# Performance work log

Hardware: AMD Instinct MI355X
Metric: run time of the kernel (lower is better)

Reference implementation:

```python
import jax, jax.numpy as jnp
import numpy as np
from jax import lax

# NARX hyperparameters (match init_kwargs)
D_I, D_O, D_X, D_Y, D_HL = 8, 8, 32, 16, 256
B, T = 2048, 512
IN_SIZE = D_I * D_X + D_O * D_Y  # 384


def setup_inputs() -> dict:
    key = jax.random.key(0)
    k1, k2, k3, k4, k5 = jax.random.split(key, 5)
    s1 = 1.0 / np.sqrt(IN_SIZE).astype(np.float32)
    s2 = 1.0 / np.sqrt(D_HL).astype(np.float32)
    x = jax.random.normal(k1, (B, T, D_X), dtype=jnp.float32)
    W1 = jax.random.uniform(k2, (D_HL, IN_SIZE), jnp.float32, -s1, s1)
    b1 = jax.random.uniform(k3, (D_HL,), jnp.float32, -s1, s1)
    W2 = jax.random.uniform(k4, (D_Y, D_HL), jnp.float32, -s2, s2)
    b2 = jax.random.uniform(k5, (D_Y,), jnp.float32, -s2, s2)
    return {"x": x, "W1": W1, "b1": b1, "W2": W2, "b2": b2}


def reference(x, W1, b1, W2, b2):
    # Closed-loop NARX: mode='close', y=None, bootstrap=None.
    # y_pred starts as zeros; loop runs from max(d_i, d_o) to T.
    Bb, Tt, _ = x.shape
    start = max(D_I, D_O)

    def step(hist, t):
        # hist: [B, d_o, d_y], oldest first == y_pred[:, t-d_o:t, :]
        xw = lax.dynamic_slice_in_dim(x, t - D_I, D_I, axis=1).reshape(Bb, D_I * D_X)
        inp = jnp.concatenate([xw, hist.reshape(Bb, D_O * D_Y)], axis=1)
        h = jnp.tanh(inp @ W1.T + b1)
        out = jax.nn.sigmoid(h @ W2.T + b2)  # act2 = Sigmoid
        new_hist = jnp.concatenate([hist[:, 1:, :], out[:, None, :]], axis=1)
        return new_hist, out

    hist0 = jnp.zeros((Bb, D_O, D_Y), dtype=x.dtype)  # zero-initialized y_pred history
    _, outs = lax.scan(step, hist0, jnp.arange(start, Tt))
    outs = jnp.transpose(outs, (1, 0, 2))  # [B, T-start, d_y]
    prefix = jnp.zeros((Bb, start, D_Y), dtype=x.dtype)
    return jnp.concatenate([prefix, outs], axis=1)  # [B, T, d_y]
```

## Files before the change

kernel.cpp:

```cpp
#include <hip/hip_runtime.h>
#include <hip/hip_bf16.h>


typedef short bf16x8 __attribute__((ext_vector_type(8)));
typedef float f32x4  __attribute__((ext_vector_type(4)));

#define MFMA16(A,B,C) __builtin_amdgcn_mfma_f32_16x16x32_bf16((A),(B),(C),0,0,0)

constexpr int DT = 512;
constexpr int DX = 32;
constexpr int DY = 16;
constexpr int BB = 16;

constexpr int XROW  = 40;
constexpr int XSLOT = 16 * XROW;
constexpr int YROW  = 24;
constexpr int YSLOT = 16 * YROW;
constexpr int HROW  = 264;

__device__ __forceinline__ short bfbits(float f) {
  return __builtin_bit_cast(short, (__bf16)f);
}
__device__ __forceinline__ float fast_tanh(float a) {
  float e = __expf(2.0f * a);
  return 1.0f - 2.0f * __builtin_amdgcn_rcpf(e + 1.0f);
}
__device__ __forceinline__ float fast_sigmoid(float a) {
  return __builtin_amdgcn_rcpf(1.0f + __expf(-a));
}

__global__ __launch_bounds__(512, 2) void narx_kernel(
    const float* __restrict__ x,  const float* __restrict__ W1,
    const float* __restrict__ b1, const float* __restrict__ W2,
    const float* __restrict__ b2, float* __restrict__ out)
{
  __shared__ __align__(16) short xbuf[8 * XSLOT];
  __shared__ __align__(16) short ybuf[8 * YSLOT];
  __shared__ __align__(16) short hbuf[16 * HROW];

  const int tid  = threadIdx.x;
  const int lane = tid & 63;
  const int w    = tid >> 6;
  const int lm   = lane & 15;
  const int lg   = lane >> 4;
  const int b0   = blockIdx.x * BB;

  bf16x8 wf[2][12];
#pragma unroll
  for (int ti = 0; ti < 2; ++ti) {
    const int n = w * 32 + ti * 16 + lm;
#pragma unroll
    for (int c = 0; c < 12; ++c) {
      const float* p = W1 + n * 384 + c * 32 + lg * 8;
      bf16x8 v;
#pragma unroll
      for (int j = 0; j < 8; ++j) v[j] = bfbits(p[j]);
      wf[ti][c] = v;
    }
  }
  bf16x8 w2f[8];
#pragma unroll
  for (int c = 0; c < 8; ++c) {
    const float* p = W2 + lm * 256 + c * 32 + lg * 8;
    bf16x8 v;
#pragma unroll
    for (int j = 0; j < 8; ++j) v[j] = bfbits(p[j]);
    w2f[c] = v;
  }
  const float b1v0 = b1[w * 32 + lm];
  const float b1v1 = b1[w * 32 + 16 + lm];
  const float b2v  = b2[lm];

  {
    const int m = tid >> 5, off = (tid & 31) * 4;
    f32x4 z = {0.f, 0.f, 0.f, 0.f};
    *reinterpret_cast<f32x4*>(out + (size_t)(b0 + m) * (DT * DY) + off) = z;
  }

  {
    const int m = tid >> 5, k = tid & 31;
#pragma unroll
    for (int tt = 0; tt < 8; ++tt)
      xbuf[tt * XSLOT + m * XROW + k] =
          bfbits(x[(size_t)(b0 + m) * (DT * DX) + tt * DX + k]);
    for (int i = tid; i < 8 * YSLOT; i += 512) ybuf[i] = 0;
  }
  __syncthreads();

  const int pm = tid >> 5, pk = tid & 31;

  for (int t = 8; t < DT; ++t) {
    const float xv = x[(size_t)(b0 + pm) * (DT * DX) + t * DX + pk];

    bf16x8 af[12];
#pragma unroll
    for (int c = 0; c < 8; ++c) {
      const int slot = (t + c) & 7;
      af[c] = *reinterpret_cast<const bf16x8*>(
          &xbuf[slot * XSLOT + lm * XROW + lg * 8]);
    }
#pragma unroll
    for (int c = 0; c < 4; ++c) {
      const int i    = c * 2 + (lg >> 1);
      const int slot = (t + i) & 7;
      af[8 + c] = *reinterpret_cast<const bf16x8*>(
          &ybuf[slot * YSLOT + lm * YROW + (lg & 1) * 8]);
    }
    f32x4 acc0a = {0.f, 0.f, 0.f, 0.f}, acc0b = {0.f, 0.f, 0.f, 0.f};
    f32x4 acc1a = {0.f, 0.f, 0.f, 0.f}, acc1b = {0.f, 0.f, 0.f, 0.f};
#pragma unroll
    for (int c = 0; c < 6; ++c) {
      acc0a = MFMA16(af[c],     wf[0][c],     acc0a);
      acc1a = MFMA16(af[c],     wf[1][c],     acc1a);
      acc0b = MFMA16(af[c + 6], wf[0][c + 6], acc0b);
      acc1b = MFMA16(af[c + 6], wf[1][c + 6], acc1b);
    }
#pragma unroll
    for (int r = 0; r < 4; ++r) {
      const int row = lg * 4 + r;
      const float h0 = fast_tanh(acc0a[r] + acc0b[r] + b1v0);
      const float h1 = fast_tanh(acc1a[r] + acc1b[r] + b1v1);
      hbuf[row * HROW + w * 32 + lm]      = bfbits(h0);
      hbuf[row * HROW + w * 32 + 16 + lm] = bfbits(h1);
    }
    __syncthreads();

    if (w < 2) {
      f32x4 a2 = {0.f, 0.f, 0.f, 0.f};
      f32x4 a3 = {0.f, 0.f, 0.f, 0.f};
#pragma unroll
      for (int c = 0; c < 4; ++c) {
        bf16x8 hf0 = *reinterpret_cast<const bf16x8*>(
            &hbuf[lm * HROW + (2 * c) * 32 + lg * 8]);
        bf16x8 hf1 = *reinterpret_cast<const bf16x8*>(
            &hbuf[lm * HROW + (2 * c + 1) * 32 + lg * 8]);
        a2 = MFMA16(hf0, w2f[2 * c],     a2);
        a3 = MFMA16(hf1, w2f[2 * c + 1], a3);
      }
#pragma unroll
      for (int r = 0; r < 4; ++r) {
        const float o = fast_sigmoid(a2[r] + a3[r] + b2v);
        if (w == 0) {
          ybuf[(t & 7) * YSLOT + (lg * 4 + r) * YROW + lm] = bfbits(o);
        } else {
          out[(size_t)(b0 + lg * 4 + r) * (DT * DY) + t * DY + lm] = o;
        }
      }
    }
    xbuf[(t & 7) * XSLOT + pm * XROW + pk] = bfbits(xv);
    __syncthreads();
  }
}

extern "C" void kernel_launch(void* const* d_in, const int* in_sizes, int n_in,
                              void* d_out, int out_size, void* d_ws, size_t ws_size,
                              hipStream_t stream) {
  const float* x  = (const float*)d_in[0];
  const float* W1 = (const float*)d_in[1];
  const float* b1 = (const float*)d_in[2];
  const float* W2 = (const float*)d_in[3];
  const float* b2 = (const float*)d_in[4];
  float* out = (float*)d_out;
  narx_kernel<<<dim3(128), dim3(512), 0, stream>>>(x, W1, b1, W2, b2, out);
}
```

Baseline: 801.4 us.

## Split second-layer matmul across all waves with LDS partial-sum reduction

Each of the 8 waves now computes a split-K partial of the output layer with one MFMA over its own 32 hidden units, instead of two waves doing the full 256-wide product. Partials go to a padded LDS buffer, and 256 threads then sum the 8 partials, apply the sigmoid, and write both the feedback history and the output. This shortens the serial per-timestep critical path and frees registers that held the full W2 fragment set. In exchange it adds an LDS partial buffer and an 8-way reduction per step, and the final sum runs on scalar threads.

```diff
diff --git a/kernel.cpp b/kernel.cpp
--- a/kernel.cpp
+++ b/kernel.cpp
@@ -17,6 +17,8 @@
 constexpr int YROW  = 24;
 constexpr int YSLOT = 16 * YROW;
 constexpr int HROW  = 264;
+constexpr int PROW  = 17;
+constexpr int PWAVE = 16 * PROW;
 
 __device__ __forceinline__ short bfbits(float f) {
   return __builtin_bit_cast(short, (__bf16)f);
@@ -37,6 +39,7 @@
   __shared__ __align__(16) short xbuf[8 * XSLOT];
   __shared__ __align__(16) short ybuf[8 * YSLOT];
   __shared__ __align__(16) short hbuf[16 * HROW];
+  __shared__ __align__(16) float pbuf[8 * PWAVE];
 
   const int tid  = threadIdx.x;
   const int lane = tid & 63;
@@ -58,14 +61,13 @@
       wf[ti][c] = v;
     }
   }
-  bf16x8 w2f[8];
-#pragma unroll
-  for (int c = 0; c < 8; ++c) {
-    const float* p = W2 + lm * 256 + c * 32 + lg * 8;
+  bf16x8 w2fp;
+  {
+    const float* p = W2 + lm * 256 + w * 32 + lg * 8;
     bf16x8 v;
 #pragma unroll
     for (int j = 0; j < 8; ++j) v[j] = bfbits(p[j]);
-    w2f[c] = v;
+    w2fp = v;
   }
   const float b1v0 = b1[w * 32 + lm];
   const float b1v1 = b1[w * 32 + 16 + lm];
@@ -123,29 +125,25 @@
       hbuf[row * HROW + w * 32 + lm]      = bfbits(h0);
       hbuf[row * HROW + w * 32 + 16 + lm] = bfbits(h1);
     }
+
+    bf16x8 ha = *reinterpret_cast<const bf16x8*>(
+        &hbuf[lm * HROW + w * 32 + lg * 8]);
+    f32x4 zero = {0.f, 0.f, 0.f, 0.f};
+    f32x4 part = MFMA16(ha, w2fp, zero);
+#pragma unroll
+    for (int r = 0; r < 4; ++r)
+      pbuf[w * PWAVE + (lg * 4 + r) * PROW + lm] = part[r];
     __syncthreads();
 
-    if (w < 2) {
-      f32x4 a2 = {0.f, 0.f, 0.f, 0.f};
-      f32x4 a3 = {0.f, 0.f, 0.f, 0.f};
+    if (tid < 256) {
+      const int row = tid >> 4, col = tid & 15;
+      float s = b2v;
 #pragma unroll
-      for (int c = 0; c < 4; ++c) {
-        bf16x8 hf0 = *reinterpret_cast<const bf16x8*>(
-            &hbuf[lm * HROW + (2 * c) * 32 + lg * 8]);
-        bf16x8 hf1 = *reinterpret_cast<const bf16x8*>(
-            &hbuf[lm * HROW + (2 * c + 1) * 32 + lg * 8]);
-        a2 = MFMA16(hf0, w2f[2 * c],     a2);
-        a3 = MFMA16(hf1, w2f[2 * c + 1], a3);
-      }
-#pragma unroll
-      for (int r = 0; r < 4; ++r) {
-        const float o = fast_sigmoid(a2[r] + a3[r] + b2v);
-        if (w == 0) {
-          ybuf[(t & 7) * YSLOT + (lg * 4 + r) * YROW + lm] = bfbits(o);
-        } else {
-          out[(size_t)(b0 + lg * 4 + r) * (DT * DY) + t * DY + lm] = o;
-        }
-      }
+      for (int ww = 0; ww < 8; ++ww)
+        s += pbuf[ww * PWAVE + row * PROW + col];
+      const float o = fast_sigmoid(s);
+      ybuf[(t & 7) * YSLOT + row * YROW + col] = bfbits(o);
+      out[(size_t)(b0 + row) * (DT * DY) + t * DY + col] = o;
     }
     xbuf[(t & 7) * XSLOT + pm * XROW + pk] = bfbits(xv);
     __syncthreads();
```

Measured after the change: 765.6 us. -4.5%, faster.
